# Optimization experiments

Hardware: AMD Instinct MI355X
Metric: run time of the kernel (lower is better)

Reference implementation:

```python
import jax, jax.numpy as jnp
import numpy as np

ORDER = 8
POOL = 8
N_SIDE = 1 << ORDER          # 256
N_PIX = N_SIDE * N_SIDE      # 65536
PSQ = POOL * POOL            # 64
CHANNEL = 2 * PSQ            # 128
PATH_NUM = N_PIX // PSQ      # 1024


def hilbert_indices(order):
    """hil[d] = row-major pixel index of the d-th point on the Hilbert curve;
    rehil = inverse permutation (rehil[hil[d]] = d)."""
    n = 1 << order
    d = np.arange(n * n, dtype=np.int64)
    x = np.zeros_like(d)
    y = np.zeros_like(d)
    t = d.copy()
    s = 1
    while s < n:
        rx = 1 & (t // 2)
        ry = 1 & (t ^ rx)
        swap = ry == 0
        flip = swap & (rx == 1)
        x = np.where(flip, s - 1 - x, x)
        y = np.where(flip, s - 1 - y, y)
        x, y = np.where(swap, y, x), np.where(swap, x, y)
        x = x + s * rx
        y = y + s * ry
        t = t // 4
        s *= 2
    hil = (y * n + x).astype(np.int32)
    rehil = np.argsort(hil).astype(np.int32)
    return hil, rehil


def setup_inputs() -> dict:
    key = jax.random.key(0)
    ks = jax.random.split(key, 10)
    b, c = 8, 128
    scale = 1.0 / np.sqrt(CHANNEL)
    hil, rehil = hilbert_indices(ORDER)
    return {
        "x": jax.random.normal(ks[0], (b, c, N_SIDE, N_SIDE), jnp.float32),
        "Wq": jax.random.normal(ks[1], (CHANNEL, CHANNEL), jnp.float32) * scale,
        "bq": jax.random.normal(ks[2], (CHANNEL,), jnp.float32) * 0.01,
        "Wk": jax.random.normal(ks[3], (CHANNEL, CHANNEL), jnp.float32) * scale,
        "bk": jax.random.normal(ks[4], (CHANNEL,), jnp.float32) * 0.01,
        "Wv": jax.random.normal(ks[5], (CHANNEL, CHANNEL), jnp.float32) * scale,
        "bv": jax.random.normal(ks[6], (CHANNEL,), jnp.float32) * 0.01,
        "Wpre": jax.random.normal(ks[7], (1, 2), jnp.float32) * 0.5,
        "bpre": jax.random.normal(ks[8], (1,), jnp.float32) * 0.01,
        "hil": jnp.asarray(hil),
        "rehil": jnp.asarray(rehil),
    }


def reference(x, Wq, bq, Wk, bk, Wv, bv, Wpre, bpre, hil, rehil):
    b, c, h, w = x.shape
    n_pix = h * w
    psq = Wq.shape[0] // 2
    path_num = n_pix // psq

    # channel-pooled descriptor: (b, 2, h*w)
    mean = jnp.mean(x, axis=1)
    mx = jnp.max(x, axis=1)
    x1 = jnp.stack([mean, mx], axis=1).reshape(b, 2, n_pix)

    # Hilbert-curve gather reorder of pixels
    xh = x1[:, :, hil]                                            # (b, 2, n_pix)

    # group psq consecutive curve points into one token of dim 2*psq
    feat = xh.reshape(b, 2, path_num, psq)
    feat = feat.transpose(0, 1, 3, 2).reshape(b, 2 * psq, path_num)  # (b, C, P)

    # 1x1-conv QKV projections
    Q = jnp.einsum('oc,bcp->bop', Wq, feat) + bq[None, :, None]
    K = jnp.einsum('oc,bcp->bop', Wk, feat) + bk[None, :, None]
    V = jnp.einsum('oc,bcp->bop', Wv, feat) + bv[None, :, None]

    # scores[b,p,q] = sum_c Q[b,c,p] * K[b,c,q]; softmax over dim 1 (as nn.Softmax(1))
    scores = jnp.einsum('bcp,bcq->bpq', Q, K)
    a = jax.nn.softmax(scores, axis=1)

    # x3c[b,c,p] = sum_q a[b,p,q] * V[b,c,q]
    x3c = jnp.einsum('bpq,bcq->bcp', a, V)                        # (b, C, P)

    # ungroup tokens back to curve order, then inverse-Hilbert scatter
    back = x3c.reshape(b, 2, psq, path_num).transpose(0, 1, 3, 2).reshape(b, 2, n_pix)
    restored = back[:, :, rehil].reshape(b, 2, h, w)

    # 1x1 conv 2 -> 1, sigmoid gate
    att = jnp.einsum('oc,bchw->bohw', Wpre, restored) + bpre[None, :, None, None]
    return jax.nn.sigmoid(att) * x
```

## Files before the change

### kernel.cpp

```cpp
#include <hip/hip_runtime.h>

#define BATCH 8
#define CH 128
#define NPIX 65536
#define PN 1024

__global__ __launch_bounds__(256) void k0_precompute(
    const float* __restrict__ Wq, const float* __restrict__ bq,
    const float* __restrict__ Wk, const float* __restrict__ bk,
    float* __restrict__ M, float* __restrict__ wqbk,
    float* __restrict__ wkbq, float* __restrict__ c0) {
  int t = blockIdx.x * 256 + threadIdx.x;
  if (t < 16384) {
    int c = t >> 7, c2 = t & 127;
    float s = 0.f;
    for (int o = 0; o < 128; ++o) s += Wq[o * 128 + c] * Wk[o * 128 + c2];
    M[t] = s;
  } else if (t < 16512) {
    int c = t - 16384;
    float s = 0.f;
    for (int o = 0; o < 128; ++o) s += Wq[o * 128 + c] * bk[o];
    wqbk[c] = s;
  } else if (t < 16640) {
    int c = t - 16512;
    float s = 0.f;
    for (int o = 0; o < 128; ++o) s += bq[o] * Wk[o * 128 + c];
    wkbq[c] = s;
  } else if (t == 16640) {
    float s = 0.f;
    for (int o = 0; o < 128; ++o) s += bq[o] * bk[o];
    c0[0] = s;
  }
}

__global__ __launch_bounds__(256) void k1_reduce_permute(
    const float* __restrict__ x, const int* __restrict__ rehil,
    float* __restrict__ F) {
  const int b = blockIdx.y;
  const int t = blockIdx.x * 256 + threadIdx.x;
  const int i0 = t * 4;
  const float* xb = x + (size_t)b * CH * NPIX + i0;
  float4 s = make_float4(0.f, 0.f, 0.f, 0.f);
  float4 m = make_float4(-1e30f, -1e30f, -1e30f, -1e30f);
  for (int c = 0; c < CH; ++c) {
    const float4 v = *(const float4*)(xb + (size_t)c * NPIX);
    s.x += v.x; s.y += v.y; s.z += v.z; s.w += v.w;
    m.x = fmaxf(m.x, v.x); m.y = fmaxf(m.y, v.y);
    m.z = fmaxf(m.z, v.z); m.w = fmaxf(m.w, v.w);
  }
  const float inv = 1.f / (float)CH;
  float mean[4] = {s.x * inv, s.y * inv, s.z * inv, s.w * inv};
  float mx[4] = {m.x, m.y, m.z, m.w};
  const int4 d4 = *(const int4*)(rehil + i0);
  int ds[4] = {d4.x, d4.y, d4.z, d4.w};
  float* Fb = F + (size_t)b * CH * PN;
#pragma unroll
  for (int e = 0; e < 4; ++e) {
    int d = ds[e];
    int p = d >> 6, j = d & 63;
    Fb[j * PN + p] = mean[e];
    Fb[(64 + j) * PN + p] = mx[e];
  }
}

__global__ __launch_bounds__(256) void ku_uv(
    const float* __restrict__ F, const float* __restrict__ wqbk,
    const float* __restrict__ wkbq, float* __restrict__ u, float* __restrict__ v) {
  const int b = blockIdx.y;
  const int p = blockIdx.x * 256 + threadIdx.x;
  const float* Fb = F + (size_t)b * CH * PN;
  float su = 0.f, sv = 0.f;
  for (int c = 0; c < CH; ++c) {
    float f = Fb[c * PN + p];
    su = fmaf(f, wqbk[c], su);
    sv = fmaf(f, wkbq[c], sv);
  }
  u[b * PN + p] = su;
  v[b * PN + p] = sv;
}

__global__ __launch_bounds__(256) void k2_gv(
    const float* __restrict__ M, const float* __restrict__ Wv,
    const float* __restrict__ bv, const float* __restrict__ F,
    float* __restrict__ G, float* __restrict__ Vt) {
  __shared__ float As[16][64];
  __shared__ float Bs[16][64];
  const int b = blockIdx.z;
  const int r0 = blockIdx.y * 64;
  const int q0 = blockIdx.x * 64;
  const float* Fb = F + (size_t)b * CH * PN;
  const int t = threadIdx.x;
  const int tx = t & 15, ty = t >> 4;
  const int arow = t & 63, ak4 = (t >> 6) * 4;
  float acc[4][4] = {};
  for (int k0 = 0; k0 < 128; k0 += 16) {
    const int r = r0 + arow;
    const float* Arow = (r < 128) ? (M + r * 128) : (Wv + (r - 128) * 128);
    float4 a = *(const float4*)(Arow + k0 + ak4);
    As[ak4 + 0][arow] = a.x;
    As[ak4 + 1][arow] = a.y;
    As[ak4 + 2][arow] = a.z;
    As[ak4 + 3][arow] = a.w;
    *(float4*)&Bs[ty][tx * 4] =
        *(const float4*)(Fb + (size_t)(k0 + ty) * PN + q0 + tx * 4);
    __syncthreads();
#pragma unroll
    for (int kk = 0; kk < 16; ++kk) {
      float4 a4 = *(const float4*)&As[kk][ty * 4];
      float4 b4 = *(const float4*)&Bs[kk][tx * 4];
      float av[4] = {a4.x, a4.y, a4.z, a4.w};
      float bw[4] = {b4.x, b4.y, b4.z, b4.w};
#pragma unroll
      for (int i = 0; i < 4; ++i)
#pragma unroll
        for (int j = 0; j < 4; ++j) acc[i][j] = fmaf(av[i], bw[j], acc[i][j]);
    }
    __syncthreads();
  }
  float* Gb = G + (size_t)b * CH * PN;
  float* Vtb = Vt + (size_t)b * PN * CH;
#pragma unroll
  for (int i = 0; i < 4; ++i) {
    const int r = r0 + ty * 4 + i;
#pragma unroll
    for (int j = 0; j < 4; ++j) {
      const int q = q0 + tx * 4 + j;
      if (r < 128) Gb[r * PN + q] = acc[i][j];
      else Vtb[(size_t)q * CH + (r - 128)] = acc[i][j] + bv[r - 128];
    }
  }
}

__global__ __launch_bounds__(256) void k3_scores(
    const float* __restrict__ G, const float* __restrict__ F,
    const float* __restrict__ u, const float* __restrict__ v,
    const float* __restrict__ c0, float* __restrict__ St) {
  __shared__ float As[16][64];
  __shared__ float Bs[16][64];
  const int b = blockIdx.z;
  const int q0 = blockIdx.y * 64;
  const int p0 = blockIdx.x * 64;
  const float* Gb = G + (size_t)b * CH * PN;
  const float* Fb = F + (size_t)b * CH * PN;
  const int t = threadIdx.x;
  const int tx = t & 15, ty = t >> 4;
  float acc[4][4] = {};
  for (int k0 = 0; k0 < 128; k0 += 16) {
    *(float4*)&As[ty][tx * 4] =
        *(const float4*)(Gb + (size_t)(k0 + ty) * PN + q0 + tx * 4);
    *(float4*)&Bs[ty][tx * 4] =
        *(const float4*)(Fb + (size_t)(k0 + ty) * PN + p0 + tx * 4);
    __syncthreads();
#pragma unroll
    for (int kk = 0; kk < 16; ++kk) {
      float4 a4 = *(const float4*)&As[kk][ty * 4];
      float4 b4 = *(const float4*)&Bs[kk][tx * 4];
      float av[4] = {a4.x, a4.y, a4.z, a4.w};
      float bw[4] = {b4.x, b4.y, b4.z, b4.w};
#pragma unroll
      for (int i = 0; i < 4; ++i)
#pragma unroll
        for (int j = 0; j < 4; ++j) acc[i][j] = fmaf(av[i], bw[j], acc[i][j]);
    }
    __syncthreads();
  }
  const float cc = c0[0];
  float* Sb = St + (size_t)b * PN * PN;
#pragma unroll
  for (int i = 0; i < 4; ++i) {
    const int q = q0 + ty * 4 + i;
    const float vq = v[b * PN + q] + cc;
#pragma unroll
    for (int j = 0; j < 4; ++j) {
      const int p = p0 + tx * 4 + j;
      Sb[(size_t)q * PN + p] = acc[i][j] + u[b * PN + p] + vq;
    }
  }
}

__global__ __launch_bounds__(256) void k4_softmax_stats(
    const float* __restrict__ St, float* __restrict__ mOut,
    float* __restrict__ izOut) {
  const int wid = threadIdx.x >> 6;
  const int lane = threadIdx.x & 63;
  const int row = blockIdx.x * 4 + wid;
  const float* Sr = St + (size_t)row * PN;
  float4 r[4];
  float m = -1e30f;
#pragma unroll
  for (int ch = 0; ch < 4; ++ch) {
    r[ch] = *(const float4*)(Sr + ch * 256 + lane * 4);
    m = fmaxf(m, fmaxf(fmaxf(r[ch].x, r[ch].y), fmaxf(r[ch].z, r[ch].w)));
  }
#pragma unroll
  for (int off = 32; off >= 1; off >>= 1) m = fmaxf(m, __shfl_xor(m, off));
  float z = 0.f;
#pragma unroll
  for (int ch = 0; ch < 4; ++ch) {
    z += __expf(r[ch].x - m) + __expf(r[ch].y - m) +
         __expf(r[ch].z - m) + __expf(r[ch].w - m);
  }
#pragma unroll
  for (int off = 32; off >= 1; off >>= 1) z += __shfl_xor(z, off);
  if (lane == 0) {
    mOut[row] = m;
    izOut[row] = 1.f / z;
  }
}

__global__ __launch_bounds__(256) void k5_av(
    const float* __restrict__ Vt, const float* __restrict__ St,
    const float* __restrict__ mIn, const float* __restrict__ izIn,
    float* __restrict__ X3) {
  __shared__ float As[16][64];
  __shared__ float Bs[16][64];
  const int b = blockIdx.z;
  const int c0 = blockIdx.y * 64;
  const int p0 = blockIdx.x * 64;
  const float* Vtb = Vt + (size_t)b * PN * CH;
  const float* Sb = St + (size_t)b * PN * PN;
  const int t = threadIdx.x;
  const int tx = t & 15, ty = t >> 4;
  float acc[4][4] = {};
  for (int k0 = 0; k0 < PN; k0 += 16) {
    const int q = k0 + ty;
    *(float4*)&As[ty][tx * 4] =
        *(const float4*)(Vtb + (size_t)q * CH + c0 + tx * 4);
    const float mq = mIn[b * PN + q];
    const float iz = izIn[b * PN + q];
    const float4 sv = *(const float4*)(Sb + (size_t)q * PN + p0 + tx * 4);
    float4 ev;
    ev.x = __expf(sv.x - mq) * iz;
    ev.y = __expf(sv.y - mq) * iz;
    ev.z = __expf(sv.z - mq) * iz;
    ev.w = __expf(sv.w - mq) * iz;
    *(float4*)&Bs[ty][tx * 4] = ev;
    __syncthreads();
#pragma unroll
    for (int kk = 0; kk < 16; ++kk) {
      float4 a4 = *(const float4*)&As[kk][ty * 4];
      float4 b4 = *(const float4*)&Bs[kk][tx * 4];
      float av[4] = {a4.x, a4.y, a4.z, a4.w};
      float bw[4] = {b4.x, b4.y, b4.z, b4.w};
#pragma unroll
      for (int i = 0; i < 4; ++i)
#pragma unroll
        for (int j = 0; j < 4; ++j) acc[i][j] = fmaf(av[i], bw[j], acc[i][j]);
    }
    __syncthreads();
  }
  float* X3b = X3 + (size_t)b * CH * PN;
#pragma unroll
  for (int i = 0; i < 4; ++i)
#pragma unroll
    for (int j = 0; j < 4; ++j)
      X3b[(size_t)(c0 + ty * 4 + i) * PN + p0 + tx * 4 + j] = acc[i][j];
}

__global__ __launch_bounds__(256) void k7_out(
    const float* __restrict__ x, const int* __restrict__ rehil,
    const float* __restrict__ X3, const float* __restrict__ Wpre,
    const float* __restrict__ bpre, float* __restrict__ out) {
  const int b = blockIdx.y;
  const int t = blockIdx.x * 256 + threadIdx.x;
  const int i0 = t * 4;
  const float w0 = Wpre[0], w1 = Wpre[1], b0 = bpre[0];
  const int4 d4 = *(const int4*)(rehil + i0);
  const float* X3b = X3 + (size_t)b * CH * PN;
  int ds[4] = {d4.x, d4.y, d4.z, d4.w};
  float g[4];
#pragma unroll
  for (int e = 0; e < 4; ++e) {
    const int d = ds[e];
    const int p = d >> 6, j = d & 63;
    const float r0v = X3b[j * PN + p];
    const float r1v = X3b[(64 + j) * PN + p];
    const float logit = fmaf(w0, r0v, fmaf(w1, r1v, b0));
    g[e] = 1.f / (1.f + __expf(-logit));
  }
  const size_t base = (size_t)b * CH * NPIX + i0;
#pragma unroll 4
  for (int c = 0; c < CH; ++c) {
    const float4 v = *(const float4*)(x + base + (size_t)c * NPIX);
    float4 o;
    o.x = v.x * g[0];
    o.y = v.y * g[1];
    o.z = v.z * g[2];
    o.w = v.w * g[3];
    *(float4*)(out + base + (size_t)c * NPIX) = o;
  }
}

extern "C" void kernel_launch(void* const* d_in, const int* in_sizes, int n_in,
                              void* d_out, int out_size, void* d_ws,
                              size_t ws_size, hipStream_t stream) {
  const float* x = (const float*)d_in[0];
  const float* Wq = (const float*)d_in[1];
  const float* bq = (const float*)d_in[2];
  const float* Wk = (const float*)d_in[3];
  const float* bk = (const float*)d_in[4];
  const float* Wv = (const float*)d_in[5];
  const float* bv = (const float*)d_in[6];
  const float* Wpre = (const float*)d_in[7];
  const float* bpre = (const float*)d_in[8];
  const int* rehil = (const int*)d_in[10];
  float* out = (float*)d_out;
  float* ws = (float*)d_ws;

  const size_t SZ_FEAT = (size_t)BATCH * CH * PN;
  float* F = ws;
  float* G = F + SZ_FEAT;
  float* Vt = G + SZ_FEAT;
  float* X3 = Vt + SZ_FEAT;
  float* Mw = X3 + SZ_FEAT;
  float* wqbk = Mw + 16384;
  float* wkbq = wqbk + 128;
  float* c0w = wkbq + 128;
  float* uw = c0w + 64;
  float* vw = uw + 8192;
  float* mw = vw + 8192;
  float* izw = mw + 8192;
  float* Stw = izw + 8192;
  const size_t need = (size_t)(Stw - ws) + (size_t)BATCH * PN * PN;
  float* St = Stw;
  if (ws_size < need * sizeof(float)) {
    St = out;
  }

  k0_precompute<<<66, 256, 0, stream>>>(Wq, bq, Wk, bk, Mw, wqbk, wkbq, c0w);
  k1_reduce_permute<<<dim3(64, BATCH), 256, 0, stream>>>(x, rehil, F);
  ku_uv<<<dim3(4, BATCH), 256, 0, stream>>>(F, wqbk, wkbq, uw, vw);
  k2_gv<<<dim3(16, 4, BATCH), 256, 0, stream>>>(Mw, Wv, bv, F, G, Vt);
  k3_scores<<<dim3(16, 16, BATCH), 256, 0, stream>>>(G, F, uw, vw, c0w, St);
  k4_softmax_stats<<<2048, 256, 0, stream>>>(St, mw, izw);
  k5_av<<<dim3(16, 2, BATCH), 256, 0, stream>>>(Vt, St, mw, izw, X3);
  k7_out<<<dim3(64, BATCH), 256, 0, stream>>>(x, rehil, X3, Wpre, bpre, out);
}
```

Before: 684.6 us.

## Fuse softmax stats into scores, split-K attention-value GEMM, fold u/v into GV GEMM

Computes the u/v bias dot products as two extra rows of the GV GEMM, removing the separate ku_uv kernel. The scores kernel now emits per-tile row max and sum-exp partials, and a small combine kernel merges them, so the full score matrix is no longer re-read just for softmax stats. The AV kernel is restructured to split the q dimension into four chunks, with an 8x4 register tile, double-buffered shared memory and all 128 channels per block. A reduce kernel then sums the four partials. This adds partial-buffer traffic and an extra launch in exchange for more parallelism and less repeated St reading.

```diff
diff --git a/kernel.cpp b/kernel.cpp
--- a/kernel.cpp
+++ b/kernel.cpp
@@ -63,26 +63,12 @@
   }
 }
 
-__global__ __launch_bounds__(256) void ku_uv(
-    const float* __restrict__ F, const float* __restrict__ wqbk,
-    const float* __restrict__ wkbq, float* __restrict__ u, float* __restrict__ v) {
-  const int b = blockIdx.y;
-  const int p = blockIdx.x * 256 + threadIdx.x;
-  const float* Fb = F + (size_t)b * CH * PN;
-  float su = 0.f, sv = 0.f;
-  for (int c = 0; c < CH; ++c) {
-    float f = Fb[c * PN + p];
-    su = fmaf(f, wqbk[c], su);
-    sv = fmaf(f, wkbq[c], sv);
-  }
-  u[b * PN + p] = su;
-  v[b * PN + p] = sv;
-}
-
 __global__ __launch_bounds__(256) void k2_gv(
     const float* __restrict__ M, const float* __restrict__ Wv,
-    const float* __restrict__ bv, const float* __restrict__ F,
-    float* __restrict__ G, float* __restrict__ Vt) {
+    const float* __restrict__ bv, const float* __restrict__ wqbk,
+    const float* __restrict__ wkbq, const float* __restrict__ F,
+    float* __restrict__ G, float* __restrict__ Vt,
+    float* __restrict__ u, float* __restrict__ v) {
   __shared__ float As[16][64];
   __shared__ float Bs[16][64];
   const int b = blockIdx.z;
@@ -95,7 +81,9 @@
   float acc[4][4] = {};
   for (int k0 = 0; k0 < 128; k0 += 16) {
     const int r = r0 + arow;
-    const float* Arow = (r < 128) ? (M + r * 128) : (Wv + (r - 128) * 128);
+    const float* Arow = (r < 128)   ? (M + r * 128)
+                        : (r < 256) ? (Wv + (r - 128) * 128)
+                        : (r == 256) ? wqbk : wkbq;
     float4 a = *(const float4*)(Arow + k0 + ak4);
     As[ak4 + 0][arow] = a.x;
     As[ak4 + 1][arow] = a.y;
@@ -126,7 +114,9 @@
     for (int j = 0; j < 4; ++j) {
       const int q = q0 + tx * 4 + j;
       if (r < 128) Gb[r * PN + q] = acc[i][j];
-      else Vtb[(size_t)q * CH + (r - 128)] = acc[i][j] + bv[r - 128];
+      else if (r < 256) Vtb[(size_t)q * CH + (r - 128)] = acc[i][j] + bv[r - 128];
+      else if (r == 256) u[b * PN + q] = acc[i][j];
+      else if (r == 257) v[b * PN + q] = acc[i][j];
     }
   }
 }
@@ -134,7 +124,8 @@
 __global__ __launch_bounds__(256) void k3_scores(
     const float* __restrict__ G, const float* __restrict__ F,
     const float* __restrict__ u, const float* __restrict__ v,
-    const float* __restrict__ c0, float* __restrict__ St) {
+    const float* __restrict__ c0, float* __restrict__ St,
+    float* __restrict__ Pm, float* __restrict__ Pz) {
   __shared__ float As[16][64];
   __shared__ float Bs[16][64];
   const int b = blockIdx.z;
@@ -165,96 +156,133 @@
     __syncthreads();
   }
   const float cc = c0[0];
+  const float4 up = *(const float4*)(u + b * PN + p0 + tx * 4);
+  const float uv[4] = {up.x, up.y, up.z, up.w};
   float* Sb = St + (size_t)b * PN * PN;
+  float* Pmb = Pm + ((size_t)b * 16 + blockIdx.x) * PN;
+  float* Pzb = Pz + ((size_t)b * 16 + blockIdx.x) * PN;
 #pragma unroll
   for (int i = 0; i < 4; ++i) {
     const int q = q0 + ty * 4 + i;
     const float vq = v[b * PN + q] + cc;
-#pragma unroll
-    for (int j = 0; j < 4; ++j) {
-      const int p = p0 + tx * 4 + j;
-      Sb[(size_t)q * PN + p] = acc[i][j] + u[b * PN + p] + vq;
-    }
-  }
-}
-
-__global__ __launch_bounds__(256) void k4_softmax_stats(
-    const float* __restrict__ St, float* __restrict__ mOut,
-    float* __restrict__ izOut) {
-  const int wid = threadIdx.x >> 6;
-  const int lane = threadIdx.x & 63;
-  const int row = blockIdx.x * 4 + wid;
-  const float* Sr = St + (size_t)row * PN;
-  float4 r[4];
+    float s[4];
+#pragma unroll
+    for (int j = 0; j < 4; ++j) s[j] = acc[i][j] + uv[j] + vq;
+    *(float4*)(Sb + (size_t)q * PN + p0 + tx * 4) =
+        make_float4(s[0], s[1], s[2], s[3]);
+    float rm = fmaxf(fmaxf(s[0], s[1]), fmaxf(s[2], s[3]));
+#pragma unroll
+    for (int off = 1; off <= 8; off <<= 1) rm = fmaxf(rm, __shfl_xor(rm, off));
+    float z = __expf(s[0] - rm) + __expf(s[1] - rm) +
+              __expf(s[2] - rm) + __expf(s[3] - rm);
+#pragma unroll
+    for (int off = 1; off <= 8; off <<= 1) z += __shfl_xor(z, off);
+    if (tx == 0) { Pmb[q] = rm; Pzb[q] = z; }
+  }
+}
+
+__global__ __launch_bounds__(256) void k4_combine(
+    const float* __restrict__ Pm, const float* __restrict__ Pz,
+    float* __restrict__ mOut, float* __restrict__ izOut) {
+  const int row = blockIdx.x * 256 + threadIdx.x;
+  const int b = row >> 10, q = row & 1023;
+  const float* Pmb = Pm + (size_t)b * 16 * PN + q;
+  const float* Pzb = Pz + (size_t)b * 16 * PN + q;
   float m = -1e30f;
 #pragma unroll
-  for (int ch = 0; ch < 4; ++ch) {
-    r[ch] = *(const float4*)(Sr + ch * 256 + lane * 4);
-    m = fmaxf(m, fmaxf(fmaxf(r[ch].x, r[ch].y), fmaxf(r[ch].z, r[ch].w)));
-  }
-#pragma unroll
-  for (int off = 32; off >= 1; off >>= 1) m = fmaxf(m, __shfl_xor(m, off));
+  for (int ti = 0; ti < 16; ++ti) m = fmaxf(m, Pmb[(size_t)ti * PN]);
   float z = 0.f;
 #pragma unroll
-  for (int ch = 0; ch < 4; ++ch) {
-    z += __expf(r[ch].x - m) + __expf(r[ch].y - m) +
-         __expf(r[ch].z - m) + __expf(r[ch].w - m);
-  }
-#pragma unroll
-  for (int off = 32; off >= 1; off >>= 1) z += __shfl_xor(z, off);
-  if (lane == 0) {
-    mOut[row] = m;
-    izOut[row] = 1.f / z;
-  }
-}
-
+  for (int ti = 0; ti < 16; ++ti)
+    z += Pzb[(size_t)ti * PN] * __expf(Pmb[(size_t)ti * PN] - m);
+  mOut[row] = m;
+  izOut[row] = 1.f / z;
+}
+
+#define QCHUNK 256
 __global__ __launch_bounds__(256) void k5_av(
     const float* __restrict__ Vt, const float* __restrict__ St,
     const float* __restrict__ mIn, const float* __restrict__ izIn,
-    float* __restrict__ X3) {
-  __shared__ float As[16][64];
-  __shared__ float Bs[16][64];
+    float* __restrict__ X3p) {
+  __shared__ float As[2][16][128];
+  __shared__ float Bs[2][16][64];
   const int b = blockIdx.z;
-  const int c0 = blockIdx.y * 64;
+  const int qc = blockIdx.y;
   const int p0 = blockIdx.x * 64;
+  const int qbase = qc * QCHUNK;
   const float* Vtb = Vt + (size_t)b * PN * CH;
   const float* Sb = St + (size_t)b * PN * PN;
   const int t = threadIdx.x;
   const int tx = t & 15, ty = t >> 4;
-  float acc[4][4] = {};
-  for (int k0 = 0; k0 < PN; k0 += 16) {
-    const int q = k0 + ty;
-    *(float4*)&As[ty][tx * 4] =
-        *(const float4*)(Vtb + (size_t)q * CH + c0 + tx * 4);
-    const float mq = mIn[b * PN + q];
-    const float iz = izIn[b * PN + q];
-    const float4 sv = *(const float4*)(Sb + (size_t)q * PN + p0 + tx * 4);
+
+  float4 a0, a1, s0;
+  float mq, zq;
+  auto issue = [&](int it) {
+    const int q = qbase + it * 16 + ty;
+    const float* ar = Vtb + (size_t)q * CH + tx * 4;
+    a0 = *(const float4*)(ar);
+    a1 = *(const float4*)(ar + 64);
+    s0 = *(const float4*)(Sb + (size_t)q * PN + p0 + tx * 4);
+    mq = mIn[b * PN + q];
+    zq = izIn[b * PN + q];
+  };
+  auto commit = [&](int buf) {
+    *(float4*)&As[buf][ty][tx * 4] = a0;
+    *(float4*)&As[buf][ty][64 + tx * 4] = a1;
     float4 ev;
-    ev.x = __expf(sv.x - mq) * iz;
-    ev.y = __expf(sv.y - mq) * iz;
-    ev.z = __expf(sv.z - mq) * iz;
-    ev.w = __expf(sv.w - mq) * iz;
-    *(float4*)&Bs[ty][tx * 4] = ev;
-    __syncthreads();
+    ev.x = __expf(s0.x - mq) * zq;
+    ev.y = __expf(s0.y - mq) * zq;
+    ev.z = __expf(s0.z - mq) * zq;
+    ev.w = __expf(s0.w - mq) * zq;
+    *(float4*)&Bs[buf][ty][tx * 4] = ev;
+  };
+
+  float acc[8][4] = {};
+  issue(0);
+  commit(0);
+  __syncthreads();
+  const int NIT = QCHUNK / 16;
+  for (int it = 0; it < NIT; ++it) {
+    const int cur = it & 1;
+    if (it + 1 < NIT) issue(it + 1);
 #pragma unroll
     for (int kk = 0; kk < 16; ++kk) {
-      float4 a4 = *(const float4*)&As[kk][ty * 4];
-      float4 b4 = *(const float4*)&Bs[kk][tx * 4];
-      float av[4] = {a4.x, a4.y, a4.z, a4.w};
-      float bw[4] = {b4.x, b4.y, b4.z, b4.w};
-#pragma unroll
-      for (int i = 0; i < 4; ++i)
+      float4 A0 = *(const float4*)&As[cur][kk][ty * 8];
+      float4 A1 = *(const float4*)&As[cur][kk][ty * 8 + 4];
+      float4 B0 = *(const float4*)&Bs[cur][kk][tx * 4];
+      float av[8] = {A0.x, A0.y, A0.z, A0.w, A1.x, A1.y, A1.z, A1.w};
+      float bw[4] = {B0.x, B0.y, B0.z, B0.w};
+#pragma unroll
+      for (int i = 0; i < 8; ++i)
 #pragma unroll
         for (int j = 0; j < 4; ++j) acc[i][j] = fmaf(av[i], bw[j], acc[i][j]);
     }
-    __syncthreads();
-  }
-  float* X3b = X3 + (size_t)b * CH * PN;
-#pragma unroll
-  for (int i = 0; i < 4; ++i)
-#pragma unroll
-    for (int j = 0; j < 4; ++j)
-      X3b[(size_t)(c0 + ty * 4 + i) * PN + p0 + tx * 4 + j] = acc[i][j];
+    if (it + 1 < NIT) commit(cur ^ 1);
+    __syncthreads();
+  }
+  float* X3b = X3p + ((size_t)qc * BATCH + b) * CH * PN;
+#pragma unroll
+  for (int i = 0; i < 8; ++i) {
+    const int c = ty * 8 + i;
+    *(float4*)(X3b + (size_t)c * PN + p0 + tx * 4) =
+        make_float4(acc[i][0], acc[i][1], acc[i][2], acc[i][3]);
+  }
+}
+
+__global__ __launch_bounds__(256) void k6_reduce(
+    const float* __restrict__ X3p, float* __restrict__ X3) {
+  const size_t SZ = (size_t)BATCH * CH * PN;
+  const size_t i = ((size_t)blockIdx.x * 256 + threadIdx.x) * 4;
+  float4 s0 = *(const float4*)(X3p + i);
+  float4 s1 = *(const float4*)(X3p + SZ + i);
+  float4 s2 = *(const float4*)(X3p + 2 * SZ + i);
+  float4 s3 = *(const float4*)(X3p + 3 * SZ + i);
+  float4 o;
+  o.x = s0.x + s1.x + s2.x + s3.x;
+  o.y = s0.y + s1.y + s2.y + s3.y;
+  o.z = s0.z + s1.z + s2.z + s3.z;
+  o.w = s0.w + s1.w + s2.w + s3.w;
+  *(float4*)(X3 + i) = o;
 }
 
 __global__ __launch_bounds__(256) void k7_out(
@@ -312,7 +340,8 @@
   float* G = F + SZ_FEAT;
   float* Vt = G + SZ_FEAT;
   float* X3 = Vt + SZ_FEAT;
-  float* Mw = X3 + SZ_FEAT;
+  float* X3p = X3 + SZ_FEAT;
+  float* Mw = X3p + 4 * SZ_FEAT;
   float* wqbk = Mw + 16384;
   float* wkbq = wqbk + 128;
   float* c0w = wkbq + 128;
@@ -320,7 +349,9 @@
   float* vw = uw + 8192;
   float* mw = vw + 8192;
   float* izw = mw + 8192;
-  float* Stw = izw + 8192;
+  float* Pm = izw + 8192;
+  float* Pz = Pm + 16 * 8192;
+  float* Stw = Pz + 16 * 8192;
   const size_t need = (size_t)(Stw - ws) + (size_t)BATCH * PN * PN;
   float* St = Stw;
   if (ws_size < need * sizeof(float)) {
@@ -329,10 +360,12 @@
 
   k0_precompute<<<66, 256, 0, stream>>>(Wq, bq, Wk, bk, Mw, wqbk, wkbq, c0w);
   k1_reduce_permute<<<dim3(64, BATCH), 256, 0, stream>>>(x, rehil, F);
-  ku_uv<<<dim3(4, BATCH), 256, 0, stream>>>(F, wqbk, wkbq, uw, vw);
-  k2_gv<<<dim3(16, 4, BATCH), 256, 0, stream>>>(Mw, Wv, bv, F, G, Vt);
-  k3_scores<<<dim3(16, 16, BATCH), 256, 0, stream>>>(G, F, uw, vw, c0w, St);
-  k4_softmax_stats<<<2048, 256, 0, stream>>>(St, mw, izw);
-  k5_av<<<dim3(16, 2, BATCH), 256, 0, stream>>>(Vt, St, mw, izw, X3);
+  k2_gv<<<dim3(16, 5, BATCH), 256, 0, stream>>>(Mw, Wv, bv, wqbk, wkbq, F, G,
+                                                Vt, uw, vw);
+  k3_scores<<<dim3(16, 16, BATCH), 256, 0, stream>>>(G, F, uw, vw, c0w, St, Pm,
+                                                     Pz);
+  k4_combine<<<32, 256, 0, stream>>>(Pm, Pz, mw, izw);
+  k5_av<<<dim3(16, 4, BATCH), 256, 0, stream>>>(Vt, St, mw, izw, X3p);
+  k6_reduce<<<1024, 256, 0, stream>>>(X3p, X3);
   k7_out<<<dim3(64, BATCH), 256, 0, stream>>>(x, rehil, X3, Wpre, bpre, out);
 }
```

Measured after the change: 649.2 us. 5.2% less time.
